# Performance work log

Hardware: AMD Instinct MI355X
Metric: run time of the kernel (lower is better)

Reference implementation:

```python
import jax, jax.numpy as jnp
import numpy as np
import math

D_MODEL = 2048
N_HEADS = 16
D_HEAD = D_MODEL // N_HEADS

def setup_inputs() -> dict:
    key = jax.random.key(0)
    ks = jax.random.split(key, 6)
    B, S, D = 4, 2048, D_MODEL
    scale = 1.0 / math.sqrt(D)
    x  = jax.random.normal(ks[0], (B, S, D), dtype=jnp.float32)
    Wq = jax.random.normal(ks[1], (D, D), dtype=jnp.float32) * scale
    Wk = jax.random.normal(ks[2], (D, D), dtype=jnp.float32) * scale
    Wv = jax.random.normal(ks[3], (D, D), dtype=jnp.float32) * scale
    Wo = jax.random.normal(ks[4], (D, D), dtype=jnp.float32) * scale
    bo = jax.random.normal(ks[5], (D,), dtype=jnp.float32) * 0.01
    return {"x": x, "Wq": Wq, "Wk": Wk, "Wv": Wv, "Wo": Wo, "bo": bo}

def reference(x, Wq, Wk, Wv, Wo, bo):
    B, S, D = x.shape
    H, Dh = N_HEADS, D_HEAD
    # projections (bias=False for q/k/v); torch Linear: y = x @ W^T
    q = (x @ Wq.T).reshape(B, S, H, Dh).transpose(0, 2, 1, 3)  # [B,H,S,Dh]
    k = (x @ Wk.T).reshape(B, S, H, Dh).transpose(0, 2, 1, 3)
    v = (x @ Wv.T).reshape(B, S, H, Dh).transpose(0, 2, 1, 3)
    scores = jnp.einsum('bhqd,bhkd->bhqk', q, k) / math.sqrt(Dh)  # [B,H,S,S]
    causal = jnp.tril(jnp.ones((S, S), dtype=bool))
    scores = jnp.where(causal, scores, -jnp.inf)
    attn = jax.nn.softmax(scores, axis=-1)
    # dropout p=0.0 -> identity (eval)
    out = jnp.einsum('bhqk,bhkd->bhqd', attn, v)  # [B,H,S,Dh]
    out = out.transpose(0, 2, 1, 3).reshape(B, S, D)
    return out @ Wo.T + bo
```

## Files before the change

### kernel.cpp

```cpp
#include <hip/hip_runtime.h>
#include <stdint.h>

#define D_MODEL 2048
#define NH 16
#define DH 128
#define BATCH 4
#define SEQ 2048
#define MTOT (BATCH*SEQ)
#define LDQ 6144

typedef __bf16 bf16x8 __attribute__((ext_vector_type(8)));
typedef float f32x4 __attribute__((ext_vector_type(4)));
typedef short short8 __attribute__((ext_vector_type(8)));

static __device__ __forceinline__ unsigned short f2bf(float f) {
  union { float f; unsigned int u; } v; v.f = f;
  return (unsigned short)((v.u + 0x7FFFu + ((v.u >> 16) & 1u)) >> 16);
}

#define FENCEM() asm volatile("" ::: "memory")
#define GBAR() do { FENCEM(); __builtin_amdgcn_s_barrier(); FENCEM(); } while (0)

__global__ __launch_bounds__(256) void cvt_bf16_k(const float* __restrict__ in,
                                                  unsigned short* __restrict__ out, int n) {
  int i = (blockIdx.x * 256 + threadIdx.x) * 8;
  if (i >= n) return;
  float4 a = *(const float4*)(in + i);
  float4 b = *(const float4*)(in + i + 4);
  union { unsigned short u[8]; short8 v; } o;
  o.u[0] = f2bf(a.x); o.u[1] = f2bf(a.y); o.u[2] = f2bf(a.z); o.u[3] = f2bf(a.w);
  o.u[4] = f2bf(b.x); o.u[5] = f2bf(b.y); o.u[6] = f2bf(b.z); o.u[7] = f2bf(b.w);
  *(short8*)(out + i) = o.v;
}

__global__ __launch_bounds__(256) void cvt_w_k(const float* __restrict__ w0, const float* __restrict__ w1,
                                               const float* __restrict__ w2, const float* __restrict__ w3,
                                               unsigned short* __restrict__ o0, unsigned short* __restrict__ o1,
                                               unsigned short* __restrict__ o2, unsigned short* __restrict__ o3) {
  const float* src; unsigned short* dst;
  switch (blockIdx.y) {
    case 0: src = w0; dst = o0; break;
    case 1: src = w1; dst = o1; break;
    case 2: src = w2; dst = o2; break;
    default: src = w3; dst = o3; break;
  }
  int i = (blockIdx.x * 256 + threadIdx.x) * 8;
  float4 a = *(const float4*)(src + i);
  float4 b = *(const float4*)(src + i + 4);
  union { unsigned short u[8]; short8 v; } o;
  o.u[0] = f2bf(a.x); o.u[1] = f2bf(a.y); o.u[2] = f2bf(a.z); o.u[3] = f2bf(a.w);
  o.u[4] = f2bf(b.x); o.u[5] = f2bf(b.y); o.u[6] = f2bf(b.z); o.u[7] = f2bf(b.w);
  *(short8*)(dst + i) = o.v;
}

template<bool OUT_BF16, bool ADD_BIAS>
__global__ __launch_bounds__(512, 2) void gemm256(const unsigned short* __restrict__ A,
                                                  const unsigned short* __restrict__ B,
                                                  void* __restrict__ C,
                                                  const float* __restrict__ bias,
                                                  int M, int N, int K) {
  __shared__ __align__(16) unsigned short As[2][256 * 64];
  __shared__ __align__(16) unsigned short Bs[2][256 * 64];

  const int tid = threadIdx.x;
  const int lane = tid & 63;
  const int l15 = lane & 15, l4 = lane >> 4;
  const int wid = tid >> 6;
  const int wr = wid >> 2, wc = wid & 3;

  const int gx = gridDim.x;
  const int id = blockIdx.y * gx + blockIdx.x;
  const int msl = gx >> 2;
  const int nsl = gridDim.y >> 1;
  const int xcd = id & 7;
  const int lid = id >> 3;
  const int bm = (xcd >> 1) * msl + lid / nsl;
  const int bn = (xcd & 1) * nsl + lid % nsl;

  const int NT = K >> 6;

  const int st_r = tid >> 3;
  const int st_c = (tid & 7) ^ (st_r & 7);
  const int st_ld = st_r * 64 + (tid & 7) * 8;

#define STAGE_A(t, h) do { \
  const int _b = (t) & 1; \
  _Pragma("unroll") \
  for (int _i = 0; _i < 2; ++_i) { \
    const unsigned short* _g = A + (size_t)(bm * 256 + (h) * 128 + _i * 64 + st_r) * K + (t) * 64 + st_c * 8; \
    __builtin_amdgcn_global_load_lds((const __attribute__((address_space(1))) void*)_g, \
        (__attribute__((address_space(3))) void*)(&As[_b][(h) * 8192 + _i * 4096 + st_ld]), 16, 0, 0); \
  } \
} while (0)

#define STAGE_B(t, h) do { \
  const int _b = (t) & 1; \
  _Pragma("unroll") \
  for (int _i = 0; _i < 2; ++_i) { \
    const unsigned short* _g = B + (size_t)(bn * 256 + (h) * 128 + _i * 64 + st_r) * K + (t) * 64 + st_c * 8; \
    __builtin_amdgcn_global_load_lds((const __attribute__((address_space(1))) void*)_g, \
        (__attribute__((address_space(3))) void*)(&Bs[_b][(h) * 8192 + _i * 4096 + st_ld]), 16, 0, 0); \
  } \
} while (0)

#define LDA_F(dst, bufb, mh) do { \
  _Pragma("unroll") \
  for (int _mi = 0; _mi < 4; ++_mi) { \
    int _row = wr * 128 + (mh) * 64 + _mi * 16 + l15; \
    _Pragma("unroll") \
    for (int _kk = 0; _kk < 2; ++_kk) \
      dst[_mi][_kk] = *(const bf16x8*)&As[bufb][_row * 64 + ((_kk * 4 + l4) ^ (l15 & 7)) * 8]; \
  } \
} while (0)

#define LDB_F(dst, bufb, nq) do { \
  _Pragma("unroll") \
  for (int _ni = 0; _ni < 2; ++_ni) { \
    int _row = wc * 64 + (nq) * 32 + _ni * 16 + l15; \
    _Pragma("unroll") \
    for (int _kk = 0; _kk < 2; ++_kk) \
      dst[_ni][_kk] = *(const bf16x8*)&Bs[bufb][_row * 64 + ((_kk * 4 + l4) ^ (l15 & 7)) * 8]; \
  } \
} while (0)

#define PHASE_MFMA(MH, NQ, BFR) do { \
  _Pragma("unroll") \
  for (int _mi = 0; _mi < 4; ++_mi) { \
    _Pragma("unroll") \
    for (int _ni = 0; _ni < 2; ++_ni) { \
      acc[(MH) * 4 + _mi][(NQ) * 2 + _ni] = __builtin_amdgcn_mfma_f32_16x16x32_bf16( \
          af[_mi][0], BFR[_ni][0], acc[(MH) * 4 + _mi][(NQ) * 2 + _ni], 0, 0, 0); \
      acc[(MH) * 4 + _mi][(NQ) * 2 + _ni] = __builtin_amdgcn_mfma_f32_16x16x32_bf16( \
          af[_mi][1], BFR[_ni][1], acc[(MH) * 4 + _mi][(NQ) * 2 + _ni], 0, 0, 0); \
    } \
  } \
} while (0)

  f32x4 acc[8][4] = {};

  STAGE_A(0, 0); STAGE_A(0, 1);
  STAGE_B(0, 0); STAGE_B(0, 1);
  if (NT > 1) { STAGE_A(1, 0); STAGE_A(1, 1); }
  if (NT > 1) asm volatile("s_waitcnt vmcnt(4)" ::: "memory");
  else        asm volatile("s_waitcnt vmcnt(0)" ::: "memory");
  GBAR();

  for (int t = 0; t < NT; ++t) {
    const int bufb = t & 1;
    bf16x8 af[4][2], bf0[2][2], bf1[2][2];

    LDA_F(af, bufb, 0);
    LDB_F(bf0, bufb, 0);
    LDB_F(bf1, bufb, 1);
    if (t + 1 < NT) { STAGE_B(t + 1, 0); STAGE_B(t + 1, 1); }
    __builtin_amdgcn_s_setprio(1);
    PHASE_MFMA(0, 0, bf0);
    PHASE_MFMA(0, 1, bf1);
    __builtin_amdgcn_s_setprio(0);

    LDA_F(af, bufb, 1);
    asm volatile("s_waitcnt lgkmcnt(0)" ::: "memory");
    GBAR();

    if (t + 2 < NT) { STAGE_A(t + 2, 0); STAGE_A(t + 2, 1); }
    __builtin_amdgcn_s_setprio(1);
    PHASE_MFMA(1, 1, bf1);
    PHASE_MFMA(1, 0, bf0);
    __builtin_amdgcn_s_setprio(0);
    if (t + 2 < NT) asm volatile("s_waitcnt vmcnt(4)" ::: "memory");
    else            asm volatile("s_waitcnt vmcnt(0)" ::: "memory");
    GBAR();
  }

  const int row0 = bm * 256 + wr * 128;
  const int col0 = bn * 256 + wc * 64;
#pragma unroll
  for (int mi = 0; mi < 8; ++mi) {
#pragma unroll
    for (int ni = 0; ni < 4; ++ni) {
      int col = col0 + ni * 16 + l15;
#pragma unroll
      for (int r = 0; r < 4; ++r) {
        int row = row0 + mi * 16 + l4 * 4 + r;
        float v = acc[mi][ni][r];
        if (ADD_BIAS) v += bias[col];
        if (OUT_BF16)
          ((unsigned short*)C)[(size_t)row * N + col] = f2bf(v);
        else
          ((float*)C)[(size_t)row * N + col] = v;
      }
    }
  }
#undef STAGE_A
#undef STAGE_B
#undef LDA_F
#undef LDB_F
#undef PHASE_MFMA
}

__global__ __launch_bounds__(256, 2) void attn_k(const unsigned short* __restrict__ Qp,
                                                 const unsigned short* __restrict__ Kp,
                                                 const unsigned short* __restrict__ Vp,
                                                 unsigned short* __restrict__ O) {
  __shared__ __align__(16) unsigned short Ks[2][64 * 128];
  __shared__ __align__(16) unsigned short Vt[2][128 * 64];
  __shared__ __align__(16) unsigned int   Pl[4][32 * 32];

  const int tid = threadIdx.x;
  const int lane = tid & 63;
  const int l15 = lane & 15, l4 = lane >> 4;
  const int w = tid >> 6;

  const int idx = blockIdx.y * gridDim.x + blockIdx.x;
  const int x8 = idx & 7, j = idx >> 3;
  const int bh = x8 * 8 + (j & 7);
  const int qt = 15 - (j >> 3);
  const int b = bh >> 4, h = bh & 15;

  const size_t baseI = (size_t)b * SEQ * LDQ + (size_t)h * DH;
  const size_t baseO = (size_t)b * SEQ * D_MODEL + (size_t)h * DH;
  const int qw = qt * 128 + w * 32;

  bf16x8 qf[2][4];
#pragma unroll
  for (int qg = 0; qg < 2; ++qg) {
    const unsigned short* qptr = Qp + baseI + (size_t)(qw + qg * 16 + l15) * LDQ;
#pragma unroll
    for (int kk = 0; kk < 4; ++kk)
      qf[qg][kk] = *(const bf16x8*)(qptr + kk * 32 + l4 * 8);
  }

  f32x4 acc[2][8] = {};
  float m_run[2] = {-3.4028235e38f, -3.4028235e38f};
  float lp[2] = {0.f, 0.f};
  const float SC = 0.12751743f;

  short8 vreg[4];
  const int nkt = 2 * qt + 2;

  const int vkp0 = tid >> 4, vch0 = tid & 15;
  const int vkp1 = (tid + 256) >> 4, vch1 = vch0;

#pragma unroll
  for (int it = 0; it < 4; ++it) {
    int c = tid + it * 256;
    int key = c >> 4, pos = c & 15;
    int gchunk = pos ^ (key & 7);
    const unsigned short* ga = Kp + baseI + (size_t)key * LDQ + gchunk * 8;
    __builtin_amdgcn_global_load_lds((const __attribute__((address_space(1))) void*)ga,
                                     (__attribute__((address_space(3))) void*)(&Ks[0][c * 8]),
                                     16, 0, 0);
  }
  FENCEM();
  {
    const unsigned short* gv0 = Vp + baseI + (size_t)(2 * vkp0) * LDQ + vch0 * 8;
    vreg[0] = *(const short8*)(gv0);
    vreg[1] = *(const short8*)(gv0 + LDQ);
    const unsigned short* gv1 = Vp + baseI + (size_t)(2 * vkp1) * LDQ + vch1 * 8;
    vreg[2] = *(const short8*)(gv1);
    vreg[3] = *(const short8*)(gv1 + LDQ);
  }

  for (int kt = 0; kt < nkt; ++kt) {
    const int cur = kt & 1;
    const int kv0 = kt * 64;
    const bool act = (kv0 <= qw + 31);

    asm volatile("s_waitcnt vmcnt(4)" ::: "memory");
    GBAR();

    f32x4 sacc[2][4] = {};
    if (act) {
      __builtin_amdgcn_s_setprio(1);
#pragma unroll
      for (int st = 0; st < 4; ++st) {
        int key = st * 16 + l15;
#pragma unroll
        for (int kk = 0; kk < 4; ++kk) {
          bf16x8 kf = *(const bf16x8*)&Ks[cur][key * 128 + ((kk * 32 + l4 * 8) ^ ((key & 7) << 3))];
          sacc[0][st] = __builtin_amdgcn_mfma_f32_16x16x32_bf16(kf, qf[0][kk], sacc[0][st], 0, 0, 0);
          sacc[1][st] = __builtin_amdgcn_mfma_f32_16x16x32_bf16(kf, qf[1][kk], sacc[1][st], 0, 0, 0);
        }
      }
      __builtin_amdgcn_s_setprio(0);
    }
    FENCEM();

    if (kt + 1 < nkt) {
      const int kn0 = kv0 + 64;
      const int nb = cur ^ 1;
#pragma unroll
      for (int it = 0; it < 4; ++it) {
        int c = tid + it * 256;
        int key = c >> 4, pos = c & 15;
        int gchunk = pos ^ (key & 7);
        const unsigned short* ga = Kp + baseI + (size_t)(kn0 + key) * LDQ + gchunk * 8;
        __builtin_amdgcn_global_load_lds((const __attribute__((address_space(1))) void*)ga,
                                         (__attribute__((address_space(3))) void*)(&Ks[nb][c * 8]),
                                         16, 0, 0);
      }
      asm volatile("s_waitcnt vmcnt(4)" ::: "memory");
    } else {
      asm volatile("s_waitcnt vmcnt(0)" ::: "memory");
    }

#pragma unroll
    for (int i = 0; i < 2; ++i) {
      int kp = i ? vkp1 : vkp0;
      int ch = i ? vch1 : vch0;
      union { short8 v; unsigned short u[8]; } ua, ub;
      ua.v = vreg[2 * i]; ub.v = vreg[2 * i + 1];
#pragma unroll
      for (int j2 = 0; j2 < 8; ++j2) {
        int dh = ch * 8 + j2;
        int sv = (ch ^ j2) & 7;
        unsigned val = (unsigned)ua.u[j2] | ((unsigned)ub.u[j2] << 16);
        *(unsigned int*)&Vt[cur][dh * 64 + ((2 * kp) ^ (sv << 3))] = val;
      }
    }
    if (kt + 1 < nkt) {
      const int kn0 = kv0 + 64;
      const unsigned short* gv0 = Vp + baseI + (size_t)(kn0 + 2 * vkp0) * LDQ + vch0 * 8;
      vreg[0] = *(const short8*)(gv0);
      vreg[1] = *(const short8*)(gv0 + LDQ);
      const unsigned short* gv1 = Vp + baseI + (size_t)(kn0 + 2 * vkp1) * LDQ + vch1 * 8;
      vreg[2] = *(const short8*)(gv1);
      vreg[3] = *(const short8*)(gv1 + LDQ);
    }
    __syncthreads();

    if (act) {
      const bool tail = (kv0 + 63 > qw);
      float tmax[2];
#pragma unroll
      for (int qg = 0; qg < 2; ++qg) {
        if (tail) {
          int q = qw + qg * 16 + l15;
#pragma unroll
          for (int st = 0; st < 4; ++st)
#pragma unroll
            for (int r = 0; r < 4; ++r) {
              int key = kv0 + st * 16 + l4 * 4 + r;
              if (key > q) sacc[qg][st][r] = -3.0e38f;
            }
        }
        float a0 = fmaxf(fmaxf(sacc[qg][0][0], sacc[qg][0][1]), fmaxf(sacc[qg][0][2], sacc[qg][0][3]));
        float a1 = fmaxf(fmaxf(sacc[qg][1][0], sacc[qg][1][1]), fmaxf(sacc[qg][1][2], sacc[qg][1][3]));
        float a2 = fmaxf(fmaxf(sacc[qg][2][0], sacc[qg][2][1]), fmaxf(sacc[qg][2][2], sacc[qg][2][3]));
        float a3 = fmaxf(fmaxf(sacc[qg][3][0], sacc[qg][3][1]), fmaxf(sacc[qg][3][2], sacc[qg][3][3]));
        float t = fmaxf(fmaxf(a0, a1), fmaxf(a2, a3));
        t = fmaxf(t, __shfl_xor(t, 16));
        t = fmaxf(t, __shfl_xor(t, 32));
        tmax[qg] = t;
      }
      bool grow = (tmax[0] > m_run[0] + 8.f) || (tmax[1] > m_run[1] + 8.f);
      if (__any(grow)) {
#pragma unroll
        for (int qg = 0; qg < 2; ++qg) {
          float nm = fmaxf(m_run[qg], tmax[qg]);
          float scl = __builtin_amdgcn_exp2f((m_run[qg] - nm) * SC);
          m_run[qg] = nm;
          lp[qg] *= scl;
#pragma unroll
          for (int r = 0; r < 4; ++r) {
            float srow = __shfl(scl, l4 * 4 + r);
#pragma unroll
            for (int df = 0; df < 8; ++df) acc[qg][df][r] *= srow;
          }
        }
      }
#pragma unroll
      for (int qg = 0; qg < 2; ++qg) {
        int q = qg * 16 + l15;
        float ps = 0.f;
#pragma unroll
        for (int st = 0; st < 4; ++st) {
          float p0 = __builtin_amdgcn_exp2f((sacc[qg][st][0] - m_run[qg]) * SC);
          float p1 = __builtin_amdgcn_exp2f((sacc[qg][st][1] - m_run[qg]) * SC);
          float p2 = __builtin_amdgcn_exp2f((sacc[qg][st][2] - m_run[qg]) * SC);
          float p3 = __builtin_amdgcn_exp2f((sacc[qg][st][3] - m_run[qg]) * SC);
          ps += (p0 + p1) + (p2 + p3);
          unsigned w0 = (unsigned)f2bf(p0) | ((unsigned)f2bf(p1) << 16);
          unsigned w1 = (unsigned)f2bf(p2) | ((unsigned)f2bf(p3) << 16);
          int kw0 = st * 8 + l4 * 2;
          Pl[w][q * 32 + (kw0 ^ ((q & 7) << 2))] = w0;
          Pl[w][q * 32 + ((kw0 + 1) ^ ((q & 7) << 2))] = w1;
        }
        lp[qg] += ps;
      }
      __builtin_amdgcn_s_setprio(1);
#pragma unroll
      for (int ks2 = 0; ks2 < 2; ++ks2) {
        int kwb = ks2 * 16 + l4 * 4;
        bf16x8 pa0 = *(const bf16x8*)&Pl[w][l15 * 32 + (kwb ^ ((l15 & 7) << 2))];
        bf16x8 pa1 = *(const bf16x8*)&Pl[w][(16 + l15) * 32 + (kwb ^ ((l15 & 7) << 2))];
#pragma unroll
        for (int df = 0; df < 8; ++df) {
          int dh = df * 16 + l15;
          int sv = ((dh >> 3) ^ dh) & 7;
          bf16x8 vb = *(const bf16x8*)&Vt[cur][dh * 64 + ((ks2 * 32 + l4 * 8) ^ (sv << 3))];
          acc[0][df] = __builtin_amdgcn_mfma_f32_16x16x32_bf16(pa0, vb, acc[0][df], 0, 0, 0);
          acc[1][df] = __builtin_amdgcn_mfma_f32_16x16x32_bf16(pa1, vb, acc[1][df], 0, 0, 0);
        }
      }
      __builtin_amdgcn_s_setprio(0);
    }
  }

#pragma unroll
  for (int qg = 0; qg < 2; ++qg) {
    float t = lp[qg];
    t += __shfl_xor(t, 16);
    t += __shfl_xor(t, 32);
    float linv = 1.0f / t;
#pragma unroll
    for (int r = 0; r < 4; ++r) {
      float lrow = __shfl(linv, l4 * 4 + r);
      int row = qw + qg * 16 + l4 * 4 + r;
#pragma unroll
      for (int df = 0; df < 8; ++df)
        O[baseO + (size_t)row * D_MODEL + df * 16 + l15] = f2bf(acc[qg][df][r] * lrow);
    }
  }
}

extern "C" void kernel_launch(void* const* d_in, const int* in_sizes, int n_in,
                              void* d_out, int out_size, void* d_ws, size_t ws_size,
                              hipStream_t stream) {
  const float* x  = (const float*)d_in[0];
  const float* Wq = (const float*)d_in[1];
  const float* Wk = (const float*)d_in[2];
  const float* Wv = (const float*)d_in[3];
  const float* Wo = (const float*)d_in[4];
  const float* bo = (const float*)d_in[5];
  float* out = (float*)d_out;

  unsigned short* ws = (unsigned short*)d_ws;
  const size_t XSZ = (size_t)MTOT * D_MODEL;
  const size_t WSZ = (size_t)D_MODEL * D_MODEL;
  unsigned short* xb   = ws;
  unsigned short* Wcat = xb + XSZ;
  unsigned short* Wob  = Wcat + 3 * WSZ;
  unsigned short* QKV  = Wob + WSZ;
  unsigned short* AOb  = xb;

  cvt_bf16_k<<<(int)(XSZ / 8 / 256), 256, 0, stream>>>(x, xb, (int)XSZ);
  dim3 gw((unsigned)(WSZ / 8 / 256), 4);
  cvt_w_k<<<gw, 256, 0, stream>>>(Wq, Wk, Wv, Wo,
                                  Wcat, Wcat + WSZ, Wcat + 2 * WSZ, Wob);

  dim3 gq(MTOT / 256, LDQ / 256);
  gemm256<true, false><<<gq, 512, 0, stream>>>(xb, Wcat, QKV, nullptr, MTOT, LDQ, D_MODEL);

  dim3 ga(SEQ / 128, BATCH * NH);
  attn_k<<<ga, 256, 0, stream>>>(QKV, QKV + 2048, QKV + 4096, AOb);

  dim3 gg(MTOT / 256, D_MODEL / 256);
  gemm256<false, true><<<gg, 512, 0, stream>>>(AOb, Wob, out, bo, MTOT, D_MODEL, D_MODEL);
}
```

Baseline: 390.3 us.

## Single-buffer GEMM LDS tiles and merge conversion kernels into one launch

The GEMM drops from double-buffered to single-buffered LDS tiles, halving shared memory (64KB to 32KB per block), which could allow more blocks per CU. The next tile is now loaded only after the mid-iteration barrier and waited on with vmcnt(0) at the end of each iteration, so global loads overlap with only half of the MFMA work instead of being prefetched a full stage ahead. Separately, the x and weight fp32-to-bf16 conversion kernels are fused into one launch to save a kernel launch. The loss of prefetch depth risks exposing memory latency in both GEMMs.

New measurement: 397.1 us. Within noise of the previous version (+1.7%).

```diff
diff --git a/kernel.cpp b/kernel.cpp
--- a/kernel.cpp
+++ b/kernel.cpp
@@ -21,30 +21,27 @@
 #define FENCEM() asm volatile("" ::: "memory")
 #define GBAR() do { FENCEM(); __builtin_amdgcn_s_barrier(); FENCEM(); } while (0)
 
-__global__ __launch_bounds__(256) void cvt_bf16_k(const float* __restrict__ in,
-                                                  unsigned short* __restrict__ out, int n) {
-  int i = (blockIdx.x * 256 + threadIdx.x) * 8;
-  if (i >= n) return;
-  float4 a = *(const float4*)(in + i);
-  float4 b = *(const float4*)(in + i + 4);
-  union { unsigned short u[8]; short8 v; } o;
-  o.u[0] = f2bf(a.x); o.u[1] = f2bf(a.y); o.u[2] = f2bf(a.z); o.u[3] = f2bf(a.w);
-  o.u[4] = f2bf(b.x); o.u[5] = f2bf(b.y); o.u[6] = f2bf(b.z); o.u[7] = f2bf(b.w);
-  *(short8*)(out + i) = o.v;
-}
-
-__global__ __launch_bounds__(256) void cvt_w_k(const float* __restrict__ w0, const float* __restrict__ w1,
-                                               const float* __restrict__ w2, const float* __restrict__ w3,
-                                               unsigned short* __restrict__ o0, unsigned short* __restrict__ o1,
-                                               unsigned short* __restrict__ o2, unsigned short* __restrict__ o3) {
-  const float* src; unsigned short* dst;
-  switch (blockIdx.y) {
-    case 0: src = w0; dst = o0; break;
-    case 1: src = w1; dst = o1; break;
-    case 2: src = w2; dst = o2; break;
-    default: src = w3; dst = o3; break;
-  }
-  int i = (blockIdx.x * 256 + threadIdx.x) * 8;
+__global__ __launch_bounds__(256) void cvt_all_k(const float* __restrict__ x,
+                                                 const float* __restrict__ w0, const float* __restrict__ w1,
+                                                 const float* __restrict__ w2, const float* __restrict__ w3,
+                                                 unsigned short* __restrict__ xo,
+                                                 unsigned short* __restrict__ wo_cat,
+                                                 unsigned short* __restrict__ wo_o) {
+  const size_t WSZ = (size_t)D_MODEL * D_MODEL;
+  int id = blockIdx.x;
+  const float* src; unsigned short* dst; int lo;
+  if (id < 8192) { src = x; dst = xo; lo = id; }
+  else {
+    int wsel = (id - 8192) >> 11;
+    lo = (id - 8192) & 2047;
+    switch (wsel) {
+      case 0: src = w0; dst = wo_cat; break;
+      case 1: src = w1; dst = wo_cat + WSZ; break;
+      case 2: src = w2; dst = wo_cat + 2 * WSZ; break;
+      default: src = w3; dst = wo_o; break;
+    }
+  }
+  int i = (lo * 256 + threadIdx.x) * 8;
   float4 a = *(const float4*)(src + i);
   float4 b = *(const float4*)(src + i + 4);
   union { unsigned short u[8]; short8 v; } o;
@@ -59,8 +56,8 @@
                                                   void* __restrict__ C,
                                                   const float* __restrict__ bias,
                                                   int M, int N, int K) {
-  __shared__ __align__(16) unsigned short As[2][256 * 64];
-  __shared__ __align__(16) unsigned short Bs[2][256 * 64];
+  __shared__ __align__(16) unsigned short As[256 * 64];
+  __shared__ __align__(16) unsigned short Bs[256 * 64];
 
   const int tid = threadIdx.x;
   const int lane = tid & 63;
@@ -84,42 +81,40 @@
   const int st_ld = st_r * 64 + (tid & 7) * 8;
 
 #define STAGE_A(t, h) do { \
-  const int _b = (t) & 1; \
   _Pragma("unroll") \
   for (int _i = 0; _i < 2; ++_i) { \
     const unsigned short* _g = A + (size_t)(bm * 256 + (h) * 128 + _i * 64 + st_r) * K + (t) * 64 + st_c * 8; \
     __builtin_amdgcn_global_load_lds((const __attribute__((address_space(1))) void*)_g, \
-        (__attribute__((address_space(3))) void*)(&As[_b][(h) * 8192 + _i * 4096 + st_ld]), 16, 0, 0); \
+        (__attribute__((address_space(3))) void*)(&As[(h) * 8192 + _i * 4096 + st_ld]), 16, 0, 0); \
   } \
 } while (0)
 
 #define STAGE_B(t, h) do { \
-  const int _b = (t) & 1; \
   _Pragma("unroll") \
   for (int _i = 0; _i < 2; ++_i) { \
     const unsigned short* _g = B + (size_t)(bn * 256 + (h) * 128 + _i * 64 + st_r) * K + (t) * 64 + st_c * 8; \
     __builtin_amdgcn_global_load_lds((const __attribute__((address_space(1))) void*)_g, \
-        (__attribute__((address_space(3))) void*)(&Bs[_b][(h) * 8192 + _i * 4096 + st_ld]), 16, 0, 0); \
+        (__attribute__((address_space(3))) void*)(&Bs[(h) * 8192 + _i * 4096 + st_ld]), 16, 0, 0); \
   } \
 } while (0)
 
-#define LDA_F(dst, bufb, mh) do { \
+#define LDA_F(dst, mh) do { \
   _Pragma("unroll") \
   for (int _mi = 0; _mi < 4; ++_mi) { \
     int _row = wr * 128 + (mh) * 64 + _mi * 16 + l15; \
     _Pragma("unroll") \
     for (int _kk = 0; _kk < 2; ++_kk) \
-      dst[_mi][_kk] = *(const bf16x8*)&As[bufb][_row * 64 + ((_kk * 4 + l4) ^ (l15 & 7)) * 8]; \
+      dst[_mi][_kk] = *(const bf16x8*)&As[_row * 64 + ((_kk * 4 + l4) ^ (l15 & 7)) * 8]; \
   } \
 } while (0)
 
-#define LDB_F(dst, bufb, nq) do { \
+#define LDB_F(dst, nq) do { \
   _Pragma("unroll") \
   for (int _ni = 0; _ni < 2; ++_ni) { \
     int _row = wc * 64 + (nq) * 32 + _ni * 16 + l15; \
     _Pragma("unroll") \
     for (int _kk = 0; _kk < 2; ++_kk) \
-      dst[_ni][_kk] = *(const bf16x8*)&Bs[bufb][_row * 64 + ((_kk * 4 + l4) ^ (l15 & 7)) * 8]; \
+      dst[_ni][_kk] = *(const bf16x8*)&Bs[_row * 64 + ((_kk * 4 + l4) ^ (l15 & 7)) * 8]; \
   } \
 } while (0)
 
@@ -140,35 +135,31 @@
 
   STAGE_A(0, 0); STAGE_A(0, 1);
   STAGE_B(0, 0); STAGE_B(0, 1);
-  if (NT > 1) { STAGE_A(1, 0); STAGE_A(1, 1); }
-  if (NT > 1) asm volatile("s_waitcnt vmcnt(4)" ::: "memory");
-  else        asm volatile("s_waitcnt vmcnt(0)" ::: "memory");
+  asm volatile("s_waitcnt vmcnt(0)" ::: "memory");
   GBAR();
 
   for (int t = 0; t < NT; ++t) {
-    const int bufb = t & 1;
     bf16x8 af[4][2], bf0[2][2], bf1[2][2];
 
-    LDA_F(af, bufb, 0);
-    LDB_F(bf0, bufb, 0);
-    LDB_F(bf1, bufb, 1);
-    if (t + 1 < NT) { STAGE_B(t + 1, 0); STAGE_B(t + 1, 1); }
+    LDA_F(af, 0);
+    LDB_F(bf0, 0);
+    LDB_F(bf1, 1);
     __builtin_amdgcn_s_setprio(1);
     PHASE_MFMA(0, 0, bf0);
     PHASE_MFMA(0, 1, bf1);
     __builtin_amdgcn_s_setprio(0);
 
-    LDA_F(af, bufb, 1);
+    LDA_F(af, 1);
     asm volatile("s_waitcnt lgkmcnt(0)" ::: "memory");
     GBAR();
 
-    if (t + 2 < NT) { STAGE_A(t + 2, 0); STAGE_A(t + 2, 1); }
+    if (t + 1 < NT) { STAGE_A(t + 1, 0); STAGE_A(t + 1, 1);
+                      STAGE_B(t + 1, 0); STAGE_B(t + 1, 1); }
     __builtin_amdgcn_s_setprio(1);
     PHASE_MFMA(1, 1, bf1);
     PHASE_MFMA(1, 0, bf0);
     __builtin_amdgcn_s_setprio(0);
-    if (t + 2 < NT) asm volatile("s_waitcnt vmcnt(4)" ::: "memory");
-    else            asm volatile("s_waitcnt vmcnt(0)" ::: "memory");
+    asm volatile("s_waitcnt vmcnt(0)" ::: "memory");
     GBAR();
   }
 
@@ -444,10 +435,7 @@
   unsigned short* QKV  = Wob + WSZ;
   unsigned short* AOb  = xb;
 
-  cvt_bf16_k<<<(int)(XSZ / 8 / 256), 256, 0, stream>>>(x, xb, (int)XSZ);
-  dim3 gw((unsigned)(WSZ / 8 / 256), 4);
-  cvt_w_k<<<gw, 256, 0, stream>>>(Wq, Wk, Wv, Wo,
-                                  Wcat, Wcat + WSZ, Wcat + 2 * WSZ, Wob);
+  cvt_all_k<<<16384, 256, 0, stream>>>(x, Wq, Wk, Wv, Wo, xb, Wcat, Wob);
 
   dim3 gq(MTOT / 256, LDQ / 256);
   gemm256<true, false><<<gq, 512, 0, stream>>>(xb, Wcat, QKV, nullptr, MTOT, LDQ, D_MODEL);
```
